# Optimization experiments

Measured on AMD Instinct MI355X. Metric: run time of the kernel, lower is better.

Reference implementation:

```python
import jax, jax.numpy as jnp
import numpy as np
from jax import lax

N, E = 50000, 800000
IN_DIM = 128
HID = 128
HEADS = 8
DPH = HID // HEADS
RH = 128
BETA = 0.1
GAMMA = 1.0
SVI_ITERS = 5
NUM_LAYERS = 2


def seg_lse(z, seg, n):
    # segment-wise logsumexp along axis 0; z: [E] or [E,H]
    m = jax.ops.segment_max(z, seg, num_segments=n)
    m0 = jnp.where(jnp.isfinite(m), m, 0.0)
    s = jax.ops.segment_sum(jnp.exp(z - m0[seg]), seg, num_segments=n)
    return jnp.where(s > 0, jnp.log(jnp.maximum(s, 1e-38)) + m0, -jnp.inf)


def seg_softmax(e, seg, n):
    lse = seg_lse(e, seg, n)
    return jnp.exp(e - lse[seg])


def gat_layer(h_in, W, a_src, a_dst, src, dst, n):
    h = (h_in @ W).reshape(n, HEADS, DPH)                       # [N,H,D]
    al_s = jnp.einsum('nhd,hd->nh', h, a_src)                   # [N,H]
    al_d = jnp.einsum('nhd,hd->nh', h, a_dst)
    e = jax.nn.leaky_relu(al_s[src] + al_d[dst], 0.2)           # [E,H]
    attn = seg_softmax(e, dst, n)                               # softmax over incoming edges
    out = jax.ops.segment_sum(attn[:, :, None] * h[src], dst, num_segments=n)
    return out.reshape(n, HEADS * DPH), attn.mean(-1)           # [N,HID], [E]


def mlp2(z, W1, b1, w2, b2):
    return jax.nn.relu(z @ W1 + b1) @ w2 + b2                   # [E]


def svi_hop(r, src, dst, n, has_out):
    # soft value iteration: V[s] = beta*logsumexp_e(Q_e/beta), Q_e = r_e + gamma*V[dst]
    def body(V, _):
        Q = r + GAMMA * V[dst]
        V2 = jnp.where(has_out, BETA * seg_lse(Q / BETA, src, n), 0.0)
        return V2, None
    V, _ = lax.scan(body, jnp.zeros(n, r.dtype), None, length=SVI_ITERS)
    Q = r + GAMMA * V[dst]
    logz = seg_lse(Q / BETA, src, n)
    log_pi = Q / BETA - logz[src]                               # per-edge log pi*(a|s=src)
    return Q, log_pi


def setup_inputs() -> dict:
    key = jax.random.key(0)
    ks = jax.random.split(key, 20)
    s = 0.05
    inp = {
        'x': jax.random.normal(ks[0], (N, IN_DIM), jnp.float32),
        'edge_index': jax.random.randint(ks[1], (2, E), 0, N, jnp.int64),
        'W0': jax.random.normal(ks[2], (IN_DIM, HID), jnp.float32) * s,
        'as0': jax.random.normal(ks[3], (HEADS, DPH), jnp.float32) * s,
        'ad0': jax.random.normal(ks[4], (HEADS, DPH), jnp.float32) * s,
        'W1': jax.random.normal(ks[5], (HID, HID), jnp.float32) * s,
        'as1': jax.random.normal(ks[6], (HEADS, DPH), jnp.float32) * s,
        'ad1': jax.random.normal(ks[7], (HEADS, DPH), jnp.float32) * s,
        'Ws1': jax.random.normal(ks[8], (4, RH), jnp.float32) * s,
        'bs1': jnp.zeros((RH,), jnp.float32),
        'ws2': jax.random.normal(ks[9], (RH,), jnp.float32) * s,
        'bs2': jnp.zeros((), jnp.float32),
        'Wm1': jax.random.normal(ks[10], (2 * HID, RH), jnp.float32) * s,
        'bm1': jnp.zeros((RH,), jnp.float32),
        'wm2': jax.random.normal(ks[11], (RH,), jnp.float32) * s,
        'bm2': jnp.zeros((), jnp.float32),
        'lam1': jnp.ones((), jnp.float32),
    }
    return inp


def reference(x, edge_index, W0, as0, ad0, W1, as1, ad1,
              Ws1, bs1, ws2, bs2, Wm1, bm1, wm2, bm2, lam1):
    n = x.shape[0]
    src, dst = edge_index[0], edge_index[1]

    # --- GAT encoder trajectory: hidden_per_hop = [x, h1], attn_per_hop = [a1, a2]
    h1, a1 = gat_layer(x, W0, as0, ad0, src, dst, n)
    h1 = jax.nn.elu(h1)
    h2, a2 = gat_layer(h1, W1, as1, ad1, src, dst, n)
    hidden = [x, h1]
    attn = [a1, a2]

    # --- structural per-edge features (degrees)
    ones_e = jnp.ones(src.shape[0], x.dtype)
    deg_out = jax.ops.segment_sum(ones_e, src, num_segments=n)
    deg_in = jax.ops.segment_sum(ones_e, dst, num_segments=n)
    sf = jnp.stack([deg_out[src], deg_in[dst],
                    jnp.log1p(deg_out[src]), jnp.log1p(deg_in[dst])], axis=-1)  # [E,4]
    r_str = mlp2(sf, Ws1, bs1, ws2, bs2)

    has_out = deg_out > 0

    # --- per-hop rewards: r = r_str + lambda1 * r_sem  (use_tmp=False)
    rewards = []
    for t in range(NUM_LAYERS):
        h = hidden[t]
        r_sem = mlp2(jnp.concatenate([h[src], h[dst]], axis=-1), Wm1, bm1, wm2, bm2)
        rewards.append(r_str + lam1 * r_sem)

    # --- soft value iteration per hop
    log_pi_star = [svi_hop(r, src, dst, n, has_out)[1] for r in rewards]

    # --- observed policy from attention (renormalized over outgoing edges)
    log_pi_obs = []
    for a in attn:
        la = jnp.log(a + 1e-12)
        log_pi_obs.append(la - seg_lse(la, src, n)[src])

    # --- NLL loss: sum_t scatter_add(-p_obs * log_pi*) over src, mean over nodes
    per_src_nll = jnp.zeros(n, x.dtype)
    for t in range(NUM_LAYERS):
        p = jnp.exp(log_pi_obs[t])
        per_src_nll = per_src_nll + jax.ops.segment_sum(-p * log_pi_star[t], src, num_segments=n)
    loss = per_src_nll.mean()

    # --- KL(pi_obs || pi*) anomaly score per node
    score = jnp.zeros(n, x.dtype)
    for t in range(NUM_LAYERS):
        p = jnp.exp(log_pi_obs[t])
        score = score + jax.ops.segment_sum(p * (log_pi_obs[t] - log_pi_star[t]), src, num_segments=n)

    return loss, score
```

## Files before the change

kernel.cpp:

```cpp
#include <hip/hip_runtime.h>
#include <math.h>

#define NN 50000
#define NE 800000

typedef _Float16 half8v __attribute__((ext_vector_type(8)));
typedef _Float16 half2v __attribute__((ext_vector_type(2)));
typedef float floatx4 __attribute__((ext_vector_type(4)));

__device__ __forceinline__ float sc_(float s, float m, float mn){
  return (s == 0.f) ? 0.f : s * expf(m - mn);
}
__device__ __forceinline__ void red16(float& v){
  v += __shfl_xor(v, 1, 64); v += __shfl_xor(v, 2, 64);
  v += __shfl_xor(v, 4, 64); v += __shfl_xor(v, 8, 64);
}
__device__ __forceinline__ void lse16(float& m, float& s){
  #pragma unroll
  for (int off = 1; off < 16; off <<= 1){
    float mo = __shfl_xor(m, off, 64), so = __shfl_xor(s, off, 64);
    float mn = fmaxf(m, mo);
    s = sc_(s, m, mn) + sc_(so, mo, mn); m = mn;
  }
}
__device__ __forceinline__ float dot2acc(half2v a, half2v b, float c){
#if __has_builtin(__builtin_amdgcn_fdot2)
  return __builtin_amdgcn_fdot2(a, b, c, false);
#else
  return c + (float)a[0]*(float)b[0] + (float)a[1]*(float)b[1];
#endif
}

__launch_bounds__(256)
__global__ void k_hist(const int* __restrict__ ei, int* __restrict__ cs, int* __restrict__ cd){
  int e = blockIdx.x*256 + threadIdx.x;
  if (e >= NE) return;
  atomicAdd(&cs[ei[e]], 1);
  atomicAdd(&cd[ei[NE + e]], 1);
}

__launch_bounds__(256)
__global__ void k_scan_a(const int* __restrict__ inA, const int* __restrict__ inB,
                         int* __restrict__ outA, int* __restrict__ outB,
                         int* __restrict__ partA, int* __restrict__ partB, int n){
  const int* in = blockIdx.y ? inB : inA;
  int* out = blockIdx.y ? outB : outA;
  int* part = blockIdx.y ? partB : partA;
  int i = blockIdx.x*256 + threadIdx.x;
  int v = (i < n) ? in[i] : 0;
  int lane = threadIdx.x & 63, wid = threadIdx.x >> 6;
  int x = v;
  #pragma unroll
  for (int off = 1; off < 64; off <<= 1){
    int t = __shfl_up(x, off, 64);
    if (lane >= off) x += t;
  }
  __shared__ int wsum[4];
  if (lane == 63) wsum[wid] = x;
  __syncthreads();
  int base = 0;
  #pragma unroll
  for (int w = 0; w < 4; ++w) if (w < wid) base += wsum[w];
  if (i < n) out[i] = base + x - v;
  if (threadIdx.x == 255) part[blockIdx.x] = base + x;
}

__launch_bounds__(256)
__global__ void k_scan_b(int* __restrict__ partA, int* __restrict__ partB, int np){
  int* part = blockIdx.y ? partB : partA;
  int i = threadIdx.x;
  int v = (i < np) ? part[i] : 0;
  int lane = threadIdx.x & 63, wid = threadIdx.x >> 6;
  int x = v;
  #pragma unroll
  for (int off = 1; off < 64; off <<= 1){
    int t = __shfl_up(x, off, 64);
    if (lane >= off) x += t;
  }
  __shared__ int wsum[4];
  if (lane == 63) wsum[wid] = x;
  __syncthreads();
  int base = 0;
  #pragma unroll
  for (int w = 0; w < 4; ++w) if (w < wid) base += wsum[w];
  if (i < np) part[i] = base + x - v;
}

__launch_bounds__(256)
__global__ void k_scan_c(int* __restrict__ outA, int* __restrict__ outB,
                         int* __restrict__ curA, int* __restrict__ curB,
                         const int* __restrict__ partA, const int* __restrict__ partB, int n){
  int* out = blockIdx.y ? outB : outA;
  int* cur = blockIdx.y ? curB : curA;
  const int* part = blockIdx.y ? partB : partA;
  int i = blockIdx.x*256 + threadIdx.x;
  if (i < n){
    int f = out[i] + part[blockIdx.x];
    out[i] = f;
    cur[i] = f;
  }
  if (blockIdx.x == 0 && threadIdx.x == 0) out[n] = NE;
}

__launch_bounds__(256)
__global__ void k_scatter(const int* __restrict__ ei, int* __restrict__ cur_s, int* __restrict__ cur_d,
                          int2* __restrict__ sd_csr, int2* __restrict__ sr_dord){
  int e = blockIdx.x*256 + threadIdx.x;
  if (e >= NE) return;
  int s = ei[e], d = ei[NE + e];
  int js = atomicAdd(&cur_s[s], 1);
  sd_csr[js] = make_int2(s, d);
  int jd = atomicAdd(&cur_d[d], 1);
  sr_dord[jd] = make_int2(s, js);
}

__launch_bounds__(256)
__global__ void k_deg(const int* __restrict__ row_s, const int* __restrict__ row_d,
                      unsigned char* __restrict__ d8o, unsigned char* __restrict__ d8i){
  int n = blockIdx.x*256 + threadIdx.x;
  if (n >= NN) return;
  int a = row_s[n+1] - row_s[n];
  int b = row_d[n+1] - row_d[n];
  d8o[n] = (unsigned char)(a > 127 ? 127 : a);
  d8i[n] = (unsigned char)(b > 127 ? 127 : b);
}

__launch_bounds__(256)
__global__ void k_prepw(const float* __restrict__ W0, const float* __restrict__ W1,
                        const float* __restrict__ Wm1, _Float16* __restrict__ Wt){
  int idx = blockIdx.x*256 + threadIdx.x;
  if (idx >= 4*128*128) return;
  int mat = idx >> 14, rem = idx & 16383;
  int n = rem >> 7, k = rem & 127;
  const float* src = (mat == 0) ? W0 : (mat == 1) ? W1 : (mat == 2) ? Wm1 : (Wm1 + 128*128);
  Wt[idx] = (_Float16)src[k*128 + n];
}

__launch_bounds__(256)
__global__ void k_strtab(const float* __restrict__ Ws1, const float* __restrict__ bs1,
                         const float* __restrict__ ws2, const float* __restrict__ bs2,
                         float* __restrict__ tab){
  int idx = blockIdx.x*256 + threadIdx.x;
  if (idx >= 128*128) return;
  float du = (float)(idx >> 7), di = (float)(idx & 127);
  float lo = log1pf(du), li = log1pf(di);
  float acc = 0.f;
  for (int c = 0; c < 128; ++c){
    float z = du*Ws1[c] + di*Ws1[128+c] + lo*Ws1[256+c] + li*Ws1[384+c] + bs1[c];
    acc += fmaxf(z, 0.f)*ws2[c];
  }
  tab[idx] = acc + bs2[0];
}

template<int AF16, int SECOND>
__launch_bounds__(256)
__global__ void k_gemm3(const void* __restrict__ Ap,
                        const _Float16* __restrict__ Bt0, const _Float16* __restrict__ Bt1,
                        const _Float16* __restrict__ Bt2,
                        const float* __restrict__ bm1,
                        const float* __restrict__ a_s, const float* __restrict__ a_d,
                        _Float16* __restrict__ Hout, _Float16* __restrict__ U01,
                        _Float16* __restrict__ V01,
                        float* __restrict__ alS, float* __restrict__ alD, int M){
  int wv = threadIdx.x >> 6, lane = threadIdx.x & 63;
  int m = lane & 15, q = lane >> 4;
  int row = blockIdx.x*64 + wv*16 + m;
  int arow = (row < M) ? row : (M-1);
  half8v af[4];
  if (AF16){
    const half8v* Ar = (const half8v*)((const _Float16*)Ap + (size_t)arow*128);
    #pragma unroll
    for (int kt = 0; kt < 4; ++kt) af[kt] = Ar[kt*4 + q];
  } else {
    const float* Ar = (const float*)Ap + (size_t)arow*128;
    #pragma unroll
    for (int kt = 0; kt < 4; ++kt){
      const float4* f = (const float4*)(Ar + kt*32 + q*8);
      float4 a0 = f[0], a1 = f[1];
      half8v h;
      h[0]=(_Float16)a0.x; h[1]=(_Float16)a0.y; h[2]=(_Float16)a0.z; h[3]=(_Float16)a0.w;
      h[4]=(_Float16)a1.x; h[5]=(_Float16)a1.y; h[6]=(_Float16)a1.z; h[7]=(_Float16)a1.w;
      af[kt] = h;
    }
  }
  floatx4 acc0[8], acc1[8], acc2[8];
  #pragma unroll
  for (int ct = 0; ct < 8; ++ct){
    #pragma unroll
    for (int r = 0; r < 4; ++r){ acc0[ct][r]=0.f; acc1[ct][r]=0.f; acc2[ct][r]=0.f; }
  }
  #pragma unroll
  for (int ct = 0; ct < 8; ++ct){
    const half8v* Br0 = (const half8v*)(Bt0 + (size_t)(ct*16 + m)*128);
    const half8v* Br1 = (const half8v*)(Bt1 + (size_t)(ct*16 + m)*128);
    const half8v* Br2 = (const half8v*)(Bt2 + (size_t)(ct*16 + m)*128);
    #pragma unroll
    for (int kt = 0; kt < 4; ++kt){
      acc0[ct] = __builtin_amdgcn_mfma_f32_16x16x32_f16(af[kt], Br0[kt*4 + q], acc0[ct], 0, 0, 0);
      acc1[ct] = __builtin_amdgcn_mfma_f32_16x16x32_f16(af[kt], Br1[kt*4 + q], acc1[ct], 0, 0, 0);
      acc2[ct] = __builtin_amdgcn_mfma_f32_16x16x32_f16(af[kt], Br2[kt*4 + q], acc2[ct], 0, 0, 0);
    }
  }
  int rb = blockIdx.x*64 + wv*16 + q*4;
  #pragma unroll
  for (int ct = 0; ct < 8; ++ct){
    float cs = a_s[ct*16 + m], cd = a_d[ct*16 + m];
    #pragma unroll
    for (int r = 0; r < 4; ++r){
      float ps = acc0[ct][r]*cs, pd = acc0[ct][r]*cd;
      #pragma unroll
      for (int off = 1; off < 16; off <<= 1){
        ps += __shfl_xor(ps, off, 64);
        pd += __shfl_xor(pd, off, 64);
      }
      int rr = rb + r;
      if (m == 0 && rr < M){ alS[rr*8 + ct] = ps; alD[rr*8 + ct] = pd; }
    }
  }
  #pragma unroll
  for (int ct = 0; ct < 8; ++ct){
    int col = ct*16 + m;
    float bv = bm1[col];
    #pragma unroll
    for (int r = 0; r < 4; ++r){
      int rr = rb + r;
      if (rr < M){
        if (SECOND == 0) Hout[(size_t)rr*128 + col] = (_Float16)acc0[ct][r];
        U01[(size_t)rr*256 + SECOND*128 + col] = (_Float16)(acc1[ct][r] + bv);
        V01[(size_t)rr*256 + SECOND*128 + col] = (_Float16)acc2[ct][r];
      }
    }
  }
}

template<bool AGG>
__launch_bounds__(256)
__global__ void k_att(const int* __restrict__ row_d, const int2* __restrict__ sr_dord,
                      const float* __restrict__ alS, const float* __restrict__ alD,
                      const _Float16* __restrict__ H,
                      float* __restrict__ la_csr, _Float16* __restrict__ h1){
  __shared__ float zbuf[4][64*8];
  int wv = threadIdx.x >> 6;
  int node = blockIdx.x*4 + wv;
  if (node >= NN) return;
  int lane = threadIdx.x & 63;
  int j0 = row_d[node], j1 = row_d[node+1];
  int deg = j1 - j0;
  if (deg == 0){
    if (AGG){
      half2v z; z[0] = (_Float16)0; z[1] = (_Float16)0;
      ((half2v*)(h1 + (size_t)node*128))[lane] = z;
    }
    return;
  }
  int head = lane & 7, slot = lane >> 3;
  float ad = alD[node*8 + head];
  float m = -INFINITY, ssum = 0.f;

  if (deg <= 64){
    for (int e = slot; e < deg; e += 8){
      int s = sr_dord[j0 + e].x;
      float z = alS[s*8 + head] + ad;
      z = (z >= 0.f) ? z : 0.2f*z;
      zbuf[wv][e*8 + head] = z;
      float mn = fmaxf(m, z);
      ssum = sc_(ssum, m, mn) + expf(z - mn);
      m = mn;
    }
    #pragma unroll
    for (int off = 8; off < 64; off <<= 1){
      float mo = __shfl_xor(m, off, 64);
      float so = __shfl_xor(ssum, off, 64);
      float mn = fmaxf(m, mo);
      ssum = sc_(ssum, m, mn) + sc_(so, mo, mn);
      m = mn;
    }
    float inv_s = 1.f / ssum;
    for (int e = slot; e < deg; e += 8){
      float a = expf(zbuf[wv][e*8 + head] - m) * inv_s;
      zbuf[wv][e*8 + head] = a;
      float asum = a;
      asum += __shfl_xor(asum, 1, 64);
      asum += __shfl_xor(asum, 2, 64);
      asum += __shfl_xor(asum, 4, 64);
      if (head == 0) la_csr[sr_dord[j0 + e].y] = logf(asum*0.125f + 1e-12f);
    }
    if (AGG){
      __asm__ volatile("s_waitcnt lgkmcnt(0)" ::: "memory");
      int h2 = lane >> 3;
      float ax = 0.f, ay = 0.f;
      const half2v* Hv = (const half2v*)H;
      for (int e = 0; e < deg; ++e){
        int s = sr_dord[j0 + e].x;
        float a = zbuf[wv][e*8 + h2];
        half2v hv = Hv[(size_t)s*64 + lane];
        ax += a*(float)hv[0];
        ay += a*(float)hv[1];
      }
      ax = (ax > 0.f) ? ax : expm1f(ax);
      ay = (ay > 0.f) ? ay : expm1f(ay);
      half2v o; o[0] = (_Float16)ax; o[1] = (_Float16)ay;
      ((half2v*)(h1 + (size_t)node*128))[lane] = o;
    }
  } else {
    for (int j = j0 + slot; j < j1; j += 8){
      int s = sr_dord[j].x;
      float z = alS[s*8 + head] + ad;
      z = (z >= 0.f) ? z : 0.2f*z;
      float mn = fmaxf(m, z);
      ssum = sc_(ssum, m, mn) + expf(z - mn);
      m = mn;
    }
    #pragma unroll
    for (int off = 8; off < 64; off <<= 1){
      float mo = __shfl_xor(m, off, 64);
      float so = __shfl_xor(ssum, off, 64);
      float mn = fmaxf(m, mo);
      ssum = sc_(ssum, m, mn) + sc_(so, mo, mn);
      m = mn;
    }
    float inv_s = 1.f / ssum;
    for (int j = j0 + slot; j < j1; j += 8){
      int s = sr_dord[j].x;
      float z = alS[s*8 + head] + ad;
      z = (z >= 0.f) ? z : 0.2f*z;
      float a = expf(z - m) * inv_s;
      float asum = a;
      asum += __shfl_xor(asum, 1, 64);
      asum += __shfl_xor(asum, 2, 64);
      asum += __shfl_xor(asum, 4, 64);
      if (head == 0) la_csr[sr_dord[j].y] = logf(asum*0.125f + 1e-12f);
    }
    if (AGG){
      int h2 = lane >> 3;
      float m2 = __shfl(m, h2*8, 64);
      float is2 = __shfl(inv_s, h2*8, 64);
      float ad2 = alD[node*8 + h2];
      float ax = 0.f, ay = 0.f;
      const half2v* Hv = (const half2v*)H;
      for (int j = j0; j < j1; ++j){
        int s = sr_dord[j].x;
        float z = alS[s*8 + h2] + ad2;
        z = (z >= 0.f) ? z : 0.2f*z;
        float a = expf(z - m2) * is2;
        half2v hv = Hv[(size_t)s*64 + lane];
        ax += a*(float)hv[0];
        ay += a*(float)hv[1];
      }
      ax = (ax > 0.f) ? ax : expm1f(ax);
      ay = (ay > 0.f) ? ay : expm1f(ay);
      half2v o; o[0] = (_Float16)ax; o[1] = (_Float16)ay;
      ((half2v*)(h1 + (size_t)node*128))[lane] = o;
    }
  }
}

__launch_bounds__(256)
__global__ void k_edge5(const int2* __restrict__ sd,
                        const unsigned char* __restrict__ d8o, const unsigned char* __restrict__ d8i,
                        const float* __restrict__ tab,
                        const _Float16* __restrict__ U01, const _Float16* __restrict__ V01,
                        const float* __restrict__ wm2, const float* __restrict__ bm2,
                        const float* __restrict__ lam1,
                        float* __restrict__ rcsr0, float* __restrict__ rcsr1){
  __shared__ _Float16 wml[128];
  if (threadIdx.x < 128) wml[threadIdx.x] = (_Float16)wm2[threadIdx.x];
  __syncthreads();
  int j = blockIdx.x*16 + (threadIdx.x >> 4);
  if (j >= NE) return;
  int t = threadIdx.x & 15;
  int2 sdv = sd[j];
  int s = sdv.x, d = sdv.y;
  const half8v* ur = (const half8v*)(U01 + (size_t)s*256);
  const half8v* vr = (const half8v*)(V01 + (size_t)d*256);
  half8v a = ur[t] + vr[t];
  half8v b = ur[16 + t] + vr[16 + t];
  #pragma unroll
  for (int k = 0; k < 8; ++k){
    a[k] = (a[k] > (_Float16)0) ? a[k] : (_Float16)0;
    b[k] = (b[k] > (_Float16)0) ? b[k] : (_Float16)0;
  }
  const half8v* wl = (const half8v*)wml;
  half8v w = wl[t];
  float r0 = 0.f, r1 = 0.f;
  #pragma unroll
  for (int c = 0; c < 4; ++c){
    half2v aa = {a[2*c], a[2*c+1]};
    half2v bb = {b[2*c], b[2*c+1]};
    half2v ww = {w[2*c], w[2*c+1]};
    r0 = dot2acc(aa, ww, r0);
    r1 = dot2acc(bb, ww, r1);
  }
  red16(r0); red16(r1);
  if (t == 0){
    float rstr = tab[((int)d8o[s] << 7) | (int)d8i[d]];
    float lam = lam1[0], bb2 = bm2[0];
    rcsr0[j] = 10.f*(rstr + lam*(r0 + bb2));
    rcsr1[j] = 10.f*(rstr + lam*(r1 + bb2));
  }
}

__launch_bounds__(256)
__global__ void k_svi(const int* __restrict__ row_s, const int2* __restrict__ sd,
                      const float* __restrict__ r0, const float* __restrict__ r1,
                      const float* __restrict__ V0in, const float* __restrict__ V1in,
                      float* __restrict__ out0, float* __restrict__ out1){
  int node = blockIdx.x*16 + (threadIdx.x >> 4);
  if (node >= NN) return;
  int t = threadIdx.x & 15;
  int j0 = row_s[node], j1 = row_s[node+1];
  if (j0 == j1){
    if (t == 0){ out0[node] = 0.f; out1[node] = 0.f; }
    return;
  }
  float m0 = -INFINITY, s0 = 0.f, m1 = -INFINITY, s1 = 0.f;
  for (int j = j0 + t; j < j1; j += 16){
    int d = sd[j].y;
    float q0 = r0[j] + V0in[d];
    float q1 = r1[j] + V1in[d];
    float mn0 = fmaxf(m0, q0);
    s0 = sc_(s0, m0, mn0) + expf(q0 - mn0); m0 = mn0;
    float mn1 = fmaxf(m1, q1);
    s1 = sc_(s1, m1, mn1) + expf(q1 - mn1); m1 = mn1;
  }
  lse16(m0, s0); lse16(m1, s1);
  if (t == 0){
    out0[node] = logf(s0) + m0;
    out1[node] = logf(s1) + m1;
  }
}

__launch_bounds__(256)
__global__ void k_final2(const int* __restrict__ row_s, const int2* __restrict__ sd,
                         const float* __restrict__ la0, const float* __restrict__ la1,
                         const float* __restrict__ r0, const float* __restrict__ r1,
                         const float* __restrict__ V0, const float* __restrict__ V1,
                         float* __restrict__ out, float* __restrict__ partial){
  int node = blockIdx.x*16 + (threadIdx.x >> 4);
  int t = threadIdx.x & 15;
  float nll = 0.f;
  if (node < NN){
    int j0 = row_s[node], j1 = row_s[node+1];
    int deg = j1 - j0;
    if (deg == 0){
      if (t == 0) out[1 + node] = 0.f;
    } else if (deg <= 32){
      int ja = j0 + t, jb = j0 + t + 16;
      float q0a=-INFINITY,q1a=-INFINITY,l0a=-INFINITY,l1a=-INFINITY;
      float q0b=-INFINITY,q1b=-INFINITY,l0b=-INFINITY,l1b=-INFINITY;
      if (ja < j1){
        int d = sd[ja].y;
        q0a = r0[ja] + V0[d]; q1a = r1[ja] + V1[d];
        l0a = la0[ja]; l1a = la1[ja];
      }
      if (jb < j1){
        int d = sd[jb].y;
        q0b = r0[jb] + V0[d]; q1b = r1[jb] + V1[d];
        l0b = la0[jb]; l1b = la1[jb];
      }
      float mq0 = fmaxf(q0a, q0b), mq1 = fmaxf(q1a, q1b);
      float ml0 = fmaxf(l0a, l0b), ml1 = fmaxf(l1a, l1b);
      float sq0 = 0.f, sq1 = 0.f, sl0 = 0.f, sl1 = 0.f;
      if (q0a != -INFINITY) sq0 += expf(q0a - mq0);
      if (q0b != -INFINITY) sq0 += expf(q0b - mq0);
      if (q1a != -INFINITY) sq1 += expf(q1a - mq1);
      if (q1b != -INFINITY) sq1 += expf(q1b - mq1);
      if (l0a != -INFINITY) sl0 += expf(l0a - ml0);
      if (l0b != -INFINITY) sl0 += expf(l0b - ml0);
      if (l1a != -INFINITY) sl1 += expf(l1a - ml1);
      if (l1b != -INFINITY) sl1 += expf(l1b - ml1);
      lse16(mq0, sq0); lse16(mq1, sq1); lse16(ml0, sl0); lse16(ml1, sl1);
      float L0 = logf(sq0) + mq0, L1 = logf(sq1) + mq1;
      float O0 = logf(sl0) + ml0, O1 = logf(sl1) + ml1;
      float sca = 0.f;
      if (ja < j1){
        float lp0 = l0a - O0, p0 = expf(lp0), ls0 = q0a - L0;
        nll -= p0*ls0; sca += p0*(lp0 - ls0);
        float lp1 = l1a - O1, p1 = expf(lp1), ls1 = q1a - L1;
        nll -= p1*ls1; sca += p1*(lp1 - ls1);
      }
      if (jb < j1){
        float lp0 = l0b - O0, p0 = expf(lp0), ls0 = q0b - L0;
        nll -= p0*ls0; sca += p0*(lp0 - ls0);
        float lp1 = l1b - O1, p1 = expf(lp1), ls1 = q1b - L1;
        nll -= p1*ls1; sca += p1*(lp1 - ls1);
      }
      red16(sca);
      if (t == 0) out[1 + node] = sca;
    } else {
      float mq0=-INFINITY, sq0=0.f, mq1=-INFINITY, sq1=0.f;
      float ma0=-INFINITY, sa0=0.f, ma1=-INFINITY, sa1=0.f;
      for (int j = j0 + t; j < j1; j += 16){
        int d = sd[j].y;
        float q0 = r0[j] + V0[d];
        float q1 = r1[j] + V1[d];
        float v0 = la0[j], v1 = la1[j];
        float mn;
        mn = fmaxf(mq0, q0); sq0 = sc_(sq0, mq0, mn) + expf(q0 - mn); mq0 = mn;
        mn = fmaxf(mq1, q1); sq1 = sc_(sq1, mq1, mn) + expf(q1 - mn); mq1 = mn;
        mn = fmaxf(ma0, v0); sa0 = sc_(sa0, ma0, mn) + expf(v0 - mn); ma0 = mn;
        mn = fmaxf(ma1, v1); sa1 = sc_(sa1, ma1, mn) + expf(v1 - mn); ma1 = mn;
      }
      lse16(mq0, sq0); lse16(mq1, sq1); lse16(ma0, sa0); lse16(ma1, sa1);
      float L0 = logf(sq0) + mq0, L1 = logf(sq1) + mq1;
      float O0 = logf(sa0) + ma0, O1 = logf(sa1) + ma1;
      float sca = 0.f;
      for (int j = j0 + t; j < j1; j += 16){
        int d = sd[j].y;
        float lp0 = la0[j] - O0, p0 = expf(lp0);
        float ls0 = (r0[j] + V0[d]) - L0;
        nll -= p0 * ls0;
        sca += p0 * (lp0 - ls0);
        float lp1 = la1[j] - O1, p1 = expf(lp1);
        float ls1 = (r1[j] + V1[d]) - L1;
        nll -= p1 * ls1;
        sca += p1 * (lp1 - ls1);
      }
      red16(sca);
      if (t == 0) out[1 + node] = sca;
    }
  }
  #pragma unroll
  for (int off = 1; off < 64; off <<= 1) nll += __shfl_xor(nll, off, 64);
  __shared__ float wsum[4];
  if ((threadIdx.x & 63) == 0) wsum[threadIdx.x >> 6] = nll;
  __syncthreads();
  if (threadIdx.x == 0) partial[blockIdx.x] = wsum[0]+wsum[1]+wsum[2]+wsum[3];
}

__launch_bounds__(256)
__global__ void k_nllred(const float* __restrict__ partial, int np, float* __restrict__ out){
  float s = 0.f;
  for (int i = threadIdx.x; i < np; i += 256) s += partial[i];
  #pragma unroll
  for (int off = 1; off < 64; off <<= 1) s += __shfl_xor(s, off, 64);
  __shared__ float wsum[4];
  if ((threadIdx.x & 63) == 0) wsum[threadIdx.x >> 6] = s;
  __syncthreads();
  if (threadIdx.x == 0) out[0] = (wsum[0]+wsum[1]+wsum[2]+wsum[3]) * (1.f/NN);
}

extern "C" void kernel_launch(void* const* d_in, const int* in_sizes, int n_in,
                              void* d_out, int out_size, void* d_ws, size_t ws_size,
                              hipStream_t stream){
  const float* x    = (const float*)d_in[0];
  const int*   ei   = (const int*)d_in[1];
  const float* W0   = (const float*)d_in[2];
  const float* as0  = (const float*)d_in[3];
  const float* ad0  = (const float*)d_in[4];
  const float* W1   = (const float*)d_in[5];
  const float* as1  = (const float*)d_in[6];
  const float* ad1  = (const float*)d_in[7];
  const float* Ws1  = (const float*)d_in[8];
  const float* bs1  = (const float*)d_in[9];
  const float* ws2  = (const float*)d_in[10];
  const float* bs2  = (const float*)d_in[11];
  const float* Wm1  = (const float*)d_in[12];
  const float* bm1  = (const float*)d_in[13];
  const float* wm2  = (const float*)d_in[14];
  const float* bm2  = (const float*)d_in[15];
  const float* lam1 = (const float*)d_in[16];
  float* out = (float*)d_out;

  char* p = (char*)d_ws;
  auto alloc = [&](size_t bytes)->void*{
    void* r = (void*)p;
    p += (bytes + 255) & ~(size_t)255;
    return r;
  };
  _Float16* Hh   = (_Float16*)alloc((size_t)NN*128*2);
  _Float16* h1f  = (_Float16*)alloc((size_t)NN*128*2);
  _Float16* U01  = (_Float16*)alloc((size_t)NN*256*2);
  _Float16* V01  = (_Float16*)alloc((size_t)NN*256*2);
  _Float16* Wt   = (_Float16*)alloc((size_t)4*128*128*2);
  float* tab     = (float*)alloc((size_t)128*128*4);
  int2*  sd_csr  = (int2*)alloc((size_t)NE*8);
  int2*  sr_dord = (int2*)alloc((size_t)NE*8);
  int*   row_s   = (int*)alloc((size_t)(NN+1)*4);
  int*   row_d   = (int*)alloc((size_t)(NN+1)*4);
  int*   cur_s   = (int*)alloc((size_t)NN*4);
  int*   cur_d   = (int*)alloc((size_t)NN*4);
  int*   partA   = (int*)alloc(256*4);
  int*   partB   = (int*)alloc(256*4);
  unsigned char* d8o = (unsigned char*)alloc(NN);
  unsigned char* d8i = (unsigned char*)alloc(NN);
  float* alS     = (float*)alloc((size_t)NN*8*4);
  float* alD     = (float*)alloc((size_t)NN*8*4);
  float* acsr0   = (float*)alloc((size_t)NE*4);
  float* acsr1   = (float*)alloc((size_t)NE*4);
  float* rcsr0   = (float*)alloc((size_t)NE*4);
  float* rcsr1   = (float*)alloc((size_t)NE*4);
  float* V0a = (float*)alloc((size_t)NN*4);
  float* V0b = (float*)alloc((size_t)NN*4);
  float* V1a = (float*)alloc((size_t)NN*4);
  float* V1b = (float*)alloc((size_t)NN*4);
  float* nllpart = (float*)alloc((size_t)4*((NN+15)/16 + 1));

  _Float16* W0t = Wt;
  _Float16* W1t = Wt + 128*128;
  _Float16* Wut = Wt + 2*128*128;
  _Float16* Wvt = Wt + 3*128*128;

  const int G_E    = (NE + 255)/256;
  const int G_gemm = (NN + 63)/64;
  const int G_n4   = (NN + 3)/4;
  const int G_n16  = (NN + 15)/16;
  const int G_e16  = (NE + 15)/16;
  const int NPART  = (NN + 255)/256;

  hipMemsetAsync(cur_s, 0, (size_t)NN*4, stream);
  hipMemsetAsync(cur_d, 0, (size_t)NN*4, stream);
  k_hist<<<G_E, 256, 0, stream>>>(ei, cur_s, cur_d);
  k_scan_a<<<dim3(NPART,2), 256, 0, stream>>>(cur_s, cur_d, row_s, row_d, partA, partB, NN);
  k_scan_b<<<dim3(1,2), 256, 0, stream>>>(partA, partB, NPART);
  k_scan_c<<<dim3(NPART,2), 256, 0, stream>>>(row_s, row_d, cur_s, cur_d, partA, partB, NN);
  k_scatter<<<G_E, 256, 0, stream>>>(ei, cur_s, cur_d, sd_csr, sr_dord);
  k_deg<<<(NN+255)/256, 256, 0, stream>>>(row_s, row_d, d8o, d8i);

  k_prepw<<<(4*128*128+255)/256, 256, 0, stream>>>(W0, W1, Wm1, Wt);
  k_strtab<<<(128*128+255)/256, 256, 0, stream>>>(Ws1, bs1, ws2, bs2, tab);

  k_gemm3<0,0><<<G_gemm, 256, 0, stream>>>(x, W0t, Wut, Wvt, bm1, as0, ad0,
                                           Hh, U01, V01, alS, alD, NN);
  k_att<true><<<G_n4, 256, 0, stream>>>(row_d, sr_dord, alS, alD, Hh, acsr0, h1f);

  k_gemm3<1,1><<<G_gemm, 256, 0, stream>>>(h1f, W1t, Wut, Wvt, bm1, as1, ad1,
                                           nullptr, U01, V01, alS, alD, NN);
  k_att<false><<<G_n4, 256, 0, stream>>>(row_d, sr_dord, alS, alD, nullptr, acsr1, nullptr);

  k_edge5<<<G_e16, 256, 0, stream>>>(sd_csr, d8o, d8i, tab,
                                     U01, V01, wm2, bm2, lam1, rcsr0, rcsr1);

  hipMemsetAsync(V0a, 0, (size_t)NN*4, stream);
  hipMemsetAsync(V1a, 0, (size_t)NN*4, stream);
  float* v0i = V0a; float* v0o = V0b;
  float* v1i = V1a; float* v1o = V1b;
  for (int it = 0; it < 5; ++it){
    k_svi<<<G_n16, 256, 0, stream>>>(row_s, sd_csr, rcsr0, rcsr1, v0i, v1i, v0o, v1o);
    float* t;
    t = v0i; v0i = v0o; v0o = t;
    t = v1i; v1i = v1o; v1o = t;
  }

  k_final2<<<G_n16, 256, 0, stream>>>(row_s, sd_csr, acsr0, acsr1, rcsr0, rcsr1,
                                      v0i, v1i, out, nllpart);
  k_nllred<<<1, 256, 0, stream>>>(nllpart, G_n16, out);
}
```

Measured before the change: 729.4 us.

## Split CSR arrays, merge setup kernels, make edge MLP node-centric

Replaces the packed int2 CSR arrays with separate int arrays, so kernels that need only the destination or source index read half the bytes. The edge MLP kernel is rewritten to walk each source node's CSR row and load that node's U row once, where it was loaded per edge. The weight prep, structural table and degree kernels are merged into one launch, and the histogram and scatter kernels now process several edges per thread with vector loads. The changes trade launch count and gather traffic for larger per-thread work. The node-centric edge kernel may suffer load imbalance on high-degree nodes.

After: 707.6 us. 1.03x faster.

```diff
diff --git a/kernel.cpp b/kernel.cpp
--- a/kernel.cpp
+++ b/kernel.cpp
@@ -33,10 +33,14 @@
 
 __launch_bounds__(256)
 __global__ void k_hist(const int* __restrict__ ei, int* __restrict__ cs, int* __restrict__ cd){
-  int e = blockIdx.x*256 + threadIdx.x;
-  if (e >= NE) return;
-  atomicAdd(&cs[ei[e]], 1);
-  atomicAdd(&cd[ei[NE + e]], 1);
+  int e0 = (blockIdx.x*256 + threadIdx.x)*4;
+  if (e0 >= NE) return;
+  int4 s = *(const int4*)(ei + e0);
+  int4 d = *(const int4*)(ei + NE + e0);
+  atomicAdd(&cs[s.x], 1); atomicAdd(&cs[s.y], 1);
+  atomicAdd(&cs[s.z], 1); atomicAdd(&cs[s.w], 1);
+  atomicAdd(&cd[d.x], 1); atomicAdd(&cd[d.y], 1);
+  atomicAdd(&cd[d.z], 1); atomicAdd(&cd[d.w], 1);
 }
 
 __launch_bounds__(256)
@@ -104,52 +108,57 @@
 
 __launch_bounds__(256)
 __global__ void k_scatter(const int* __restrict__ ei, int* __restrict__ cur_s, int* __restrict__ cur_d,
-                          int2* __restrict__ sd_csr, int2* __restrict__ sr_dord){
-  int e = blockIdx.x*256 + threadIdx.x;
-  if (e >= NE) return;
-  int s = ei[e], d = ei[NE + e];
-  int js = atomicAdd(&cur_s[s], 1);
-  sd_csr[js] = make_int2(s, d);
-  int jd = atomicAdd(&cur_d[d], 1);
-  sr_dord[jd] = make_int2(s, js);
-}
-
-__launch_bounds__(256)
-__global__ void k_deg(const int* __restrict__ row_s, const int* __restrict__ row_d,
-                      unsigned char* __restrict__ d8o, unsigned char* __restrict__ d8i){
-  int n = blockIdx.x*256 + threadIdx.x;
-  if (n >= NN) return;
-  int a = row_s[n+1] - row_s[n];
-  int b = row_d[n+1] - row_d[n];
-  d8o[n] = (unsigned char)(a > 127 ? 127 : a);
-  d8i[n] = (unsigned char)(b > 127 ? 127 : b);
-}
-
-__launch_bounds__(256)
-__global__ void k_prepw(const float* __restrict__ W0, const float* __restrict__ W1,
-                        const float* __restrict__ Wm1, _Float16* __restrict__ Wt){
-  int idx = blockIdx.x*256 + threadIdx.x;
-  if (idx >= 4*128*128) return;
-  int mat = idx >> 14, rem = idx & 16383;
-  int n = rem >> 7, k = rem & 127;
-  const float* src = (mat == 0) ? W0 : (mat == 1) ? W1 : (mat == 2) ? Wm1 : (Wm1 + 128*128);
-  Wt[idx] = (_Float16)src[k*128 + n];
-}
-
-__launch_bounds__(256)
-__global__ void k_strtab(const float* __restrict__ Ws1, const float* __restrict__ bs1,
-                         const float* __restrict__ ws2, const float* __restrict__ bs2,
-                         float* __restrict__ tab){
-  int idx = blockIdx.x*256 + threadIdx.x;
-  if (idx >= 128*128) return;
-  float du = (float)(idx >> 7), di = (float)(idx & 127);
-  float lo = log1pf(du), li = log1pf(di);
-  float acc = 0.f;
-  for (int c = 0; c < 128; ++c){
-    float z = du*Ws1[c] + di*Ws1[128+c] + lo*Ws1[256+c] + li*Ws1[384+c] + bs1[c];
-    acc += fmaxf(z, 0.f)*ws2[c];
-  }
-  tab[idx] = acc + bs2[0];
+                          int* __restrict__ dst_csr, int* __restrict__ src_dord,
+                          int* __restrict__ rs_dord){
+  int e0 = (blockIdx.x*256 + threadIdx.x)*2;
+  if (e0 >= NE) return;
+  int2 ss = *(const int2*)(ei + e0);
+  int2 dd = *(const int2*)(ei + NE + e0);
+  int js0 = atomicAdd(&cur_s[ss.x], 1);
+  int js1 = atomicAdd(&cur_s[ss.y], 1);
+  int jd0 = atomicAdd(&cur_d[dd.x], 1);
+  int jd1 = atomicAdd(&cur_d[dd.y], 1);
+  dst_csr[js0] = dd.x;
+  dst_csr[js1] = dd.y;
+  src_dord[jd0] = ss.x;
+  src_dord[jd1] = ss.y;
+  rs_dord[jd0] = js0;
+  rs_dord[jd1] = js1;
+}
+
+__launch_bounds__(256)
+__global__ void k_setup(const float* __restrict__ W0, const float* __restrict__ W1,
+                        const float* __restrict__ Wm1, _Float16* __restrict__ Wt,
+                        const float* __restrict__ Ws1, const float* __restrict__ bs1,
+                        const float* __restrict__ ws2, const float* __restrict__ bs2,
+                        float* __restrict__ tab,
+                        const int* __restrict__ row_s, const int* __restrict__ row_d,
+                        unsigned char* __restrict__ d8o, unsigned char* __restrict__ d8i){
+  int b = blockIdx.x;
+  if (b < 256){
+    int idx = b*256 + threadIdx.x;
+    int mat = idx >> 14, rem = idx & 16383;
+    int n = rem >> 7, k = rem & 127;
+    const float* src = (mat == 0) ? W0 : (mat == 1) ? W1 : (mat == 2) ? Wm1 : (Wm1 + 128*128);
+    Wt[idx] = (_Float16)src[k*128 + n];
+  } else if (b < 320){
+    int idx = (b - 256)*256 + threadIdx.x;
+    float du = (float)(idx >> 7), di = (float)(idx & 127);
+    float lo = log1pf(du), li = log1pf(di);
+    float acc = 0.f;
+    for (int c = 0; c < 128; ++c){
+      float z = du*Ws1[c] + di*Ws1[128+c] + lo*Ws1[256+c] + li*Ws1[384+c] + bs1[c];
+      acc += fmaxf(z, 0.f)*ws2[c];
+    }
+    tab[idx] = acc + bs2[0];
+  } else {
+    int n = (b - 320)*256 + threadIdx.x;
+    if (n >= NN) return;
+    int a = row_s[n+1] - row_s[n];
+    int c = row_d[n+1] - row_d[n];
+    d8o[n] = (unsigned char)(a > 127 ? 127 : a);
+    d8i[n] = (unsigned char)(c > 127 ? 127 : c);
+  }
 }
 
 template<int AF16, int SECOND>
@@ -235,7 +244,8 @@
 
 template<bool AGG>
 __launch_bounds__(256)
-__global__ void k_att(const int* __restrict__ row_d, const int2* __restrict__ sr_dord,
+__global__ void k_att(const int* __restrict__ row_d, const int* __restrict__ src_dord,
+                      const int* __restrict__ rs_dord,
                       const float* __restrict__ alS, const float* __restrict__ alD,
                       const _Float16* __restrict__ H,
                       float* __restrict__ la_csr, _Float16* __restrict__ h1){
@@ -259,7 +269,7 @@
 
   if (deg <= 64){
     for (int e = slot; e < deg; e += 8){
-      int s = sr_dord[j0 + e].x;
+      int s = src_dord[j0 + e];
       float z = alS[s*8 + head] + ad;
       z = (z >= 0.f) ? z : 0.2f*z;
       zbuf[wv][e*8 + head] = z;
@@ -283,7 +293,7 @@
       asum += __shfl_xor(asum, 1, 64);
       asum += __shfl_xor(asum, 2, 64);
       asum += __shfl_xor(asum, 4, 64);
-      if (head == 0) la_csr[sr_dord[j0 + e].y] = logf(asum*0.125f + 1e-12f);
+      if (head == 0) la_csr[rs_dord[j0 + e]] = logf(asum*0.125f + 1e-12f);
     }
     if (AGG){
       __asm__ volatile("s_waitcnt lgkmcnt(0)" ::: "memory");
@@ -291,7 +301,7 @@
       float ax = 0.f, ay = 0.f;
       const half2v* Hv = (const half2v*)H;
       for (int e = 0; e < deg; ++e){
-        int s = sr_dord[j0 + e].x;
+        int s = src_dord[j0 + e];
         float a = zbuf[wv][e*8 + h2];
         half2v hv = Hv[(size_t)s*64 + lane];
         ax += a*(float)hv[0];
@@ -304,7 +314,7 @@
     }
   } else {
     for (int j = j0 + slot; j < j1; j += 8){
-      int s = sr_dord[j].x;
+      int s = src_dord[j];
       float z = alS[s*8 + head] + ad;
       z = (z >= 0.f) ? z : 0.2f*z;
       float mn = fmaxf(m, z);
@@ -321,7 +331,7 @@
     }
     float inv_s = 1.f / ssum;
     for (int j = j0 + slot; j < j1; j += 8){
-      int s = sr_dord[j].x;
+      int s = src_dord[j];
       float z = alS[s*8 + head] + ad;
       z = (z >= 0.f) ? z : 0.2f*z;
       float a = expf(z - m) * inv_s;
@@ -329,7 +339,7 @@
       asum += __shfl_xor(asum, 1, 64);
       asum += __shfl_xor(asum, 2, 64);
       asum += __shfl_xor(asum, 4, 64);
-      if (head == 0) la_csr[sr_dord[j].y] = logf(asum*0.125f + 1e-12f);
+      if (head == 0) la_csr[rs_dord[j]] = logf(asum*0.125f + 1e-12f);
     }
     if (AGG){
       int h2 = lane >> 3;
@@ -339,7 +349,7 @@
       float ax = 0.f, ay = 0.f;
       const half2v* Hv = (const half2v*)H;
       for (int j = j0; j < j1; ++j){
-        int s = sr_dord[j].x;
+        int s = src_dord[j];
         float z = alS[s*8 + h2] + ad2;
         z = (z >= 0.f) ? z : 0.2f*z;
         float a = expf(z - m2) * is2;
@@ -356,7 +366,7 @@
 }
 
 __launch_bounds__(256)
-__global__ void k_edge5(const int2* __restrict__ sd,
+__global__ void k_edge6(const int* __restrict__ row_s, const int* __restrict__ dst_csr,
                         const unsigned char* __restrict__ d8o, const unsigned char* __restrict__ d8i,
                         const float* __restrict__ tab,
                         const _Float16* __restrict__ U01, const _Float16* __restrict__ V01,
@@ -366,42 +376,48 @@
   __shared__ _Float16 wml[128];
   if (threadIdx.x < 128) wml[threadIdx.x] = (_Float16)wm2[threadIdx.x];
   __syncthreads();
-  int j = blockIdx.x*16 + (threadIdx.x >> 4);
-  if (j >= NE) return;
-  int t = threadIdx.x & 15;
-  int2 sdv = sd[j];
-  int s = sdv.x, d = sdv.y;
-  const half8v* ur = (const half8v*)(U01 + (size_t)s*256);
-  const half8v* vr = (const half8v*)(V01 + (size_t)d*256);
-  half8v a = ur[t] + vr[t];
-  half8v b = ur[16 + t] + vr[16 + t];
-  #pragma unroll
-  for (int k = 0; k < 8; ++k){
-    a[k] = (a[k] > (_Float16)0) ? a[k] : (_Float16)0;
-    b[k] = (b[k] > (_Float16)0) ? b[k] : (_Float16)0;
-  }
+  int node = blockIdx.x*4 + (threadIdx.x >> 6);
+  if (node >= NN) return;
+  int lane = threadIdx.x & 63;
+  int t = lane & 15, eg = lane >> 4;
+  int j0 = row_s[node], j1 = row_s[node+1];
+  if (j0 == j1) return;
+  const half8v* ur = (const half8v*)(U01 + (size_t)node*256);
+  half8v u0 = ur[t], u1 = ur[16 + t];
   const half8v* wl = (const half8v*)wml;
   half8v w = wl[t];
-  float r0 = 0.f, r1 = 0.f;
-  #pragma unroll
-  for (int c = 0; c < 4; ++c){
-    half2v aa = {a[2*c], a[2*c+1]};
-    half2v bb = {b[2*c], b[2*c+1]};
-    half2v ww = {w[2*c], w[2*c+1]};
-    r0 = dot2acc(aa, ww, r0);
-    r1 = dot2acc(bb, ww, r1);
-  }
-  red16(r0); red16(r1);
-  if (t == 0){
-    float rstr = tab[((int)d8o[s] << 7) | (int)d8i[d]];
-    float lam = lam1[0], bb2 = bm2[0];
-    rcsr0[j] = 10.f*(rstr + lam*(r0 + bb2));
-    rcsr1[j] = 10.f*(rstr + lam*(r1 + bb2));
-  }
-}
-
-__launch_bounds__(256)
-__global__ void k_svi(const int* __restrict__ row_s, const int2* __restrict__ sd,
+  float lam = lam1[0], bb2 = bm2[0];
+  int du = (int)d8o[node] << 7;
+  for (int j = j0 + eg; j < j1; j += 4){
+    int d = dst_csr[j];
+    const half8v* vr = (const half8v*)(V01 + (size_t)d*256);
+    half8v a = u0 + vr[t];
+    half8v b = u1 + vr[16 + t];
+    #pragma unroll
+    for (int k = 0; k < 8; ++k){
+      a[k] = (a[k] > (_Float16)0) ? a[k] : (_Float16)0;
+      b[k] = (b[k] > (_Float16)0) ? b[k] : (_Float16)0;
+    }
+    float r0 = 0.f, r1 = 0.f;
+    #pragma unroll
+    for (int c = 0; c < 4; ++c){
+      half2v aa = {a[2*c], a[2*c+1]};
+      half2v bb = {b[2*c], b[2*c+1]};
+      half2v ww = {w[2*c], w[2*c+1]};
+      r0 = dot2acc(aa, ww, r0);
+      r1 = dot2acc(bb, ww, r1);
+    }
+    red16(r0); red16(r1);
+    if (t == 0){
+      float rstr = tab[du | (int)d8i[d]];
+      rcsr0[j] = 10.f*(rstr + lam*(r0 + bb2));
+      rcsr1[j] = 10.f*(rstr + lam*(r1 + bb2));
+    }
+  }
+}
+
+__launch_bounds__(256)
+__global__ void k_svi(const int* __restrict__ row_s, const int* __restrict__ dst_csr,
                       const float* __restrict__ r0, const float* __restrict__ r1,
                       const float* __restrict__ V0in, const float* __restrict__ V1in,
                       float* __restrict__ out0, float* __restrict__ out1){
@@ -415,7 +431,7 @@
   }
   float m0 = -INFINITY, s0 = 0.f, m1 = -INFINITY, s1 = 0.f;
   for (int j = j0 + t; j < j1; j += 16){
-    int d = sd[j].y;
+    int d = dst_csr[j];
     float q0 = r0[j] + V0in[d];
     float q1 = r1[j] + V1in[d];
     float mn0 = fmaxf(m0, q0);
@@ -431,7 +447,7 @@
 }
 
 __launch_bounds__(256)
-__global__ void k_final2(const int* __restrict__ row_s, const int2* __restrict__ sd,
+__global__ void k_final2(const int* __restrict__ row_s, const int* __restrict__ dst_csr,
                          const float* __restrict__ la0, const float* __restrict__ la1,
                          const float* __restrict__ r0, const float* __restrict__ r1,
                          const float* __restrict__ V0, const float* __restrict__ V1,
@@ -449,12 +465,12 @@
       float q0a=-INFINITY,q1a=-INFINITY,l0a=-INFINITY,l1a=-INFINITY;
       float q0b=-INFINITY,q1b=-INFINITY,l0b=-INFINITY,l1b=-INFINITY;
       if (ja < j1){
-        int d = sd[ja].y;
+        int d = dst_csr[ja];
         q0a = r0[ja] + V0[d]; q1a = r1[ja] + V1[d];
         l0a = la0[ja]; l1a = la1[ja];
       }
       if (jb < j1){
-        int d = sd[jb].y;
+        int d = dst_csr[jb];
         q0b = r0[jb] + V0[d]; q1b = r1[jb] + V1[d];
         l0b = la0[jb]; l1b = la1[jb];
       }
@@ -491,7 +507,7 @@
       float mq0=-INFINITY, sq0=0.f, mq1=-INFINITY, sq1=0.f;
       float ma0=-INFINITY, sa0=0.f, ma1=-INFINITY, sa1=0.f;
       for (int j = j0 + t; j < j1; j += 16){
-        int d = sd[j].y;
+        int d = dst_csr[j];
         float q0 = r0[j] + V0[d];
         float q1 = r1[j] + V1[d];
         float v0 = la0[j], v1 = la1[j];
@@ -506,7 +522,7 @@
       float O0 = logf(sa0) + ma0, O1 = logf(sa1) + ma1;
       float sca = 0.f;
       for (int j = j0 + t; j < j1; j += 16){
-        int d = sd[j].y;
+        int d = dst_csr[j];
         float lp0 = la0[j] - O0, p0 = expf(lp0);
         float ls0 = (r0[j] + V0[d]) - L0;
         nll -= p0 * ls0;
@@ -574,8 +590,9 @@
   _Float16* V01  = (_Float16*)alloc((size_t)NN*256*2);
   _Float16* Wt   = (_Float16*)alloc((size_t)4*128*128*2);
   float* tab     = (float*)alloc((size_t)128*128*4);
-  int2*  sd_csr  = (int2*)alloc((size_t)NE*8);
-  int2*  sr_dord = (int2*)alloc((size_t)NE*8);
+  int*   dst_csr = (int*)alloc((size_t)NE*4);
+  int*   src_dord= (int*)alloc((size_t)NE*4);
+  int*   rs_dord = (int*)alloc((size_t)NE*4);
   int*   row_s   = (int*)alloc((size_t)(NN+1)*4);
   int*   row_d   = (int*)alloc((size_t)(NN+1)*4);
   int*   cur_s   = (int*)alloc((size_t)NN*4);
@@ -601,48 +618,46 @@
   _Float16* Wut = Wt + 2*128*128;
   _Float16* Wvt = Wt + 3*128*128;
 
-  const int G_E    = (NE + 255)/256;
   const int G_gemm = (NN + 63)/64;
   const int G_n4   = (NN + 3)/4;
   const int G_n16  = (NN + 15)/16;
-  const int G_e16  = (NE + 15)/16;
   const int NPART  = (NN + 255)/256;
+  const int G_setup= 320 + (NN + 255)/256;
 
   hipMemsetAsync(cur_s, 0, (size_t)NN*4, stream);
   hipMemsetAsync(cur_d, 0, (size_t)NN*4, stream);
-  k_hist<<<G_E, 256, 0, stream>>>(ei, cur_s, cur_d);
+  k_hist<<<(NE/4 + 255)/256, 256, 0, stream>>>(ei, cur_s, cur_d);
   k_scan_a<<<dim3(NPART,2), 256, 0, stream>>>(cur_s, cur_d, row_s, row_d, partA, partB, NN);
   k_scan_b<<<dim3(1,2), 256, 0, stream>>>(partA, partB, NPART);
   k_scan_c<<<dim3(NPART,2), 256, 0, stream>>>(row_s, row_d, cur_s, cur_d, partA, partB, NN);
-  k_scatter<<<G_E, 256, 0, stream>>>(ei, cur_s, cur_d, sd_csr, sr_dord);
-  k_deg<<<(NN+255)/256, 256, 0, stream>>>(row_s, row_d, d8o, d8i);
-
-  k_prepw<<<(4*128*128+255)/256, 256, 0, stream>>>(W0, W1, Wm1, Wt);
-  k_strtab<<<(128*128+255)/256, 256, 0, stream>>>(Ws1, bs1, ws2, bs2, tab);
+  k_setup<<<G_setup, 256, 0, stream>>>(W0, W1, Wm1, Wt, Ws1, bs1, ws2, bs2, tab,
+                                       row_s, row_d, d8o, d8i);
+  k_scatter<<<(NE/2 + 255)/256, 256, 0, stream>>>(ei, cur_s, cur_d,
+                                                  dst_csr, src_dord, rs_dord);
 
   k_gemm3<0,0><<<G_gemm, 256, 0, stream>>>(x, W0t, Wut, Wvt, bm1, as0, ad0,
                                            Hh, U01, V01, alS, alD, NN);
-  k_att<true><<<G_n4, 256, 0, stream>>>(row_d, sr_dord, alS, alD, Hh, acsr0, h1f);
+  k_att<true><<<G_n4, 256, 0, stream>>>(row_d, src_dord, rs_dord, alS, alD, Hh, acsr0, h1f);
 
   k_gemm3<1,1><<<G_gemm, 256, 0, stream>>>(h1f, W1t, Wut, Wvt, bm1, as1, ad1,
                                            nullptr, U01, V01, alS, alD, NN);
-  k_att<false><<<G_n4, 256, 0, stream>>>(row_d, sr_dord, alS, alD, nullptr, acsr1, nullptr);
-
-  k_edge5<<<G_e16, 256, 0, stream>>>(sd_csr, d8o, d8i, tab,
-                                     U01, V01, wm2, bm2, lam1, rcsr0, rcsr1);
+  k_att<false><<<G_n4, 256, 0, stream>>>(row_d, src_dord, rs_dord, alS, alD, nullptr, acsr1, nullptr);
+
+  k_edge6<<<G_n4, 256, 0, stream>>>(row_s, dst_csr, d8o, d8i, tab,
+                                    U01, V01, wm2, bm2, lam1, rcsr0, rcsr1);
 
   hipMemsetAsync(V0a, 0, (size_t)NN*4, stream);
   hipMemsetAsync(V1a, 0, (size_t)NN*4, stream);
   float* v0i = V0a; float* v0o = V0b;
   float* v1i = V1a; float* v1o = V1b;
   for (int it = 0; it < 5; ++it){
-    k_svi<<<G_n16, 256, 0, stream>>>(row_s, sd_csr, rcsr0, rcsr1, v0i, v1i, v0o, v1o);
+    k_svi<<<G_n16, 256, 0, stream>>>(row_s, dst_csr, rcsr0, rcsr1, v0i, v1i, v0o, v1o);
     float* t;
     t = v0i; v0i = v0o; v0o = t;
     t = v1i; v1i = v1o; v1o = t;
   }
 
-  k_final2<<<G_n16, 256, 0, stream>>>(row_s, sd_csr, acsr0, acsr1, rcsr0, rcsr1,
+  k_final2<<<G_n16, 256, 0, stream>>>(row_s, dst_csr, acsr0, acsr1, rcsr0, rcsr1,
                                       v0i, v1i, out, nllpart);
   k_nllred<<<1, 256, 0, stream>>>(nllpart, G_n16, out);
 }
```
